# Kernel optimization log

Hardware: AMD Instinct MI355X
Metric: run time of the kernel (lower is better)

Reference implementation:

```python
import jax, jax.numpy as jnp
import numpy as np
from jax import lax

G, K, C_IN, C_FEAT, H, W, B = 8, 6, 512, 256, 64, 64, 1


def apply_offset(offset):
    # offset: [N, 2, H, W] pixel-space offsets -> sampling grid [N, H, W, 2] in [-1, 1]
    # channel 0 displaces x (width), channel 1 displaces y (height), matching the
    # reversed-meshgrid logic of the original torch apply_offset.
    n, _, h, w = offset.shape
    jj = jnp.arange(w, dtype=offset.dtype)[None, None, :]
    ii = jnp.arange(h, dtype=offset.dtype)[None, :, None]
    gx = (jj + offset[:, 0]) / ((w - 1.0) / 2.0) - 1.0
    gy = (ii + offset[:, 1]) / ((h - 1.0) / 2.0) - 1.0
    return jnp.stack([gx, gy], axis=-1)


def grid_sample_border(img, grid):
    # img: [N, C, H, W], grid: [N, H, W, 2] in [-1, 1]
    # Bilinear, padding_mode='border', align_corners=False (torch grid_sample default).
    n, c, h, w = img.shape
    x = jnp.clip((grid[..., 0] + 1.0) * w * 0.5 - 0.5, 0.0, w - 1.0)
    y = jnp.clip((grid[..., 1] + 1.0) * h * 0.5 - 0.5, 0.0, h - 1.0)
    x0 = jnp.floor(x)
    y0 = jnp.floor(y)
    wx = (x - x0)[:, None]  # [N,1,H,W]
    wy = (y - y0)[:, None]
    x0i = x0.astype(jnp.int32)
    y0i = y0.astype(jnp.int32)
    x1i = jnp.minimum(x0i + 1, w - 1)
    y1i = jnp.minimum(y0i + 1, h - 1)

    def gather(im, yi, xi):  # im [C,H,W]; yi, xi [H,W]
        return im[:, yi, xi]

    g = jax.vmap(gather)
    v00 = g(img, y0i, x0i)
    v01 = g(img, y0i, x1i)
    v10 = g(img, y1i, x0i)
    v11 = g(img, y1i, x1i)
    return (1.0 - wy) * ((1.0 - wx) * v00 + wx * v01) + wy * ((1.0 - wx) * v10 + wx * v11)


def setup_inputs() -> dict:
    key = jax.random.key(0)
    ks = jax.random.split(key, 11)
    s = 0.02
    return {
        "gar_feat": jax.random.normal(ks[0], (B, C_FEAT, H, W), jnp.float32),
        "cond_feat": jax.random.normal(ks[1], (B, C_FEAT, H, W), jnp.float32),
        "mask": jax.random.uniform(ks[2], (B, G, C_FEAT), dtype=jnp.float32),
        "W1": jax.random.normal(ks[3], (G, 128, C_IN, 3, 3), jnp.float32) * s,
        "b1": jax.random.normal(ks[4], (G, 128), jnp.float32) * s,
        "W2": jax.random.normal(ks[5], (G, 64, 128, 3, 3), jnp.float32) * s,
        "b2": jax.random.normal(ks[6], (G, 64), jnp.float32) * s,
        "W3": jax.random.normal(ks[7], (G, 32, 64, 3, 3), jnp.float32) * s,
        "b3": jax.random.normal(ks[8], (G, 32), jnp.float32) * s,
        "W4": jax.random.normal(ks[9], (G, 3 * K, 32, 3, 3), jnp.float32) * s,
        "b4": jax.random.normal(ks[10], (G, 3 * K), jnp.float32) * s,
    }


def reference(gar_feat, cond_feat, mask, W1, b1, W2, b2, W3, b3, W4, b4):
    b, c, h, w = gar_feat.shape
    g = W1.shape[0]
    k = W4.shape[1] // 3
    inp = jnp.concatenate([gar_feat, cond_feat], axis=1)  # [B, 2C, H, W]

    def conv(x, wgt, bias):
        return lax.conv_general_dilated(
            x, wgt, (1, 1), 'SAME', dimension_numbers=('NCHW', 'OIHW', 'NCHW')
        ) + bias[None, :, None, None]

    def lrelu(x):
        return jnp.where(x >= 0, x, 0.1 * x)

    def group_net(w1, bb1, w2, bb2, w3, bb3, w4, bb4):
        hid = lrelu(conv(inp, w1, bb1))
        hid = lrelu(conv(hid, w2, bb2))
        hid = lrelu(conv(hid, w3, bb3))
        return conv(hid, w4, bb4)  # [B, 3k, H, W]

    oa = jax.vmap(group_net)(W1, b1, W2, b2, W3, b3, W4, b4)  # [G, B, 3k, H, W]
    attn = jax.nn.softmax(oa[:, :, 2 * k:], axis=0)           # softmax across groups: [G,B,k,H,W]
    off = oa[:, :, :2 * k].reshape(g, b * k, 2, h, w)
    grid = jax.vmap(apply_offset)(off)                        # [G, B*k, H, W, 2]

    rep = jnp.repeat(gar_feat, k, axis=0)                     # [B*k, C, H, W]

    def warp_group(grid_g, attn_g, mask_g):
        samp = grid_sample_border(rep, grid_g).reshape(b, k, c, h, w)
        wfeat = jnp.sum(samp * attn_g[:, :, None], axis=1)    # [B, C, H, W]
        return wfeat * mask_g[:, :, None, None]

    warped = jax.vmap(warp_group)(grid, attn, jnp.transpose(mask, (1, 0, 2)))
    return jnp.sum(warped, axis=0)  # [B, C, H, W]
```

## Files before the change

### kernel.cpp

```cpp
#include <hip/hip_runtime.h>
#include <hip/hip_bf16.h>

typedef __hip_bfloat16 bf16;
typedef unsigned short ushort8v __attribute__((ext_vector_type(8)));
typedef short  s16x4  __attribute__((ext_vector_type(4)));
typedef short  bf16x8 __attribute__((ext_vector_type(8)));
typedef float  f32x4  __attribute__((ext_vector_type(4)));

#define HW 4096
#define IMG_W 64

__device__ __forceinline__ float bfbits2f(unsigned short u) {
    return __uint_as_float(((unsigned int)u) << 16);
}
__device__ __forceinline__ short f2bs(float f) {
    bf16 h = __float2bfloat16(f);
    return *reinterpret_cast<short*>(&h);
}

__device__ __forceinline__ void gl_lds16(const void* g, void* s) {
    __builtin_amdgcn_global_load_lds(
        (const __attribute__((address_space(1))) unsigned int*)g,
        (__attribute__((address_space(3))) unsigned int*)s, 16, 0, 0);
}

__device__ void pack_input_dev(const float* __restrict__ gar,
                               const float* __restrict__ cond,
                               short* __restrict__ outp,
                               short* __restrict__ gart, int bx2, float* tile)
{
    int bx = bx2 & 127;
    int by = bx2 >> 7;
    int tx = threadIdx.x & 31;
    int ty = threadIdx.x >> 5;
#pragma unroll
    for (int i = 0; i < 4; ++i) {
        int c = by * 32 + ty + i * 8;
        const float* src = (c < 256) ? (gar + (size_t)c * HW)
                                     : (cond + (size_t)(c - 256) * HW);
        tile[(ty + i * 8) * 33 + tx] = src[bx * 32 + tx];
    }
    __syncthreads();
#pragma unroll
    for (int i = 0; i < 4; ++i) {
        int p = bx * 32 + ty + i * 8;
        short v = f2bs(tile[tx * 33 + ty + i * 8]);
        outp[((size_t)by * 4096 + p) * 32 + tx] = v;
        if (by < 8)
            gart[(size_t)p * 256 + by * 32 + tx] = v;
    }
}

template<int CIN, int CREAL, int BN, int NT, bool COAL>
__device__ void pack_w_dev(const float* __restrict__ wgt, char* __restrict__ wp,
                           int bx, short* sT)
{
    constexpr int NCC  = CIN / 32;
    constexpr int BLKB = 9 * 4 * BN * 16;

    const int t  = threadIdx.x;
    const int cc = bx % NCC;
    const int nt = (bx / NCC) % NT;
    const int g  = bx / (NT * NCC);

    for (int i = t; i < BLKB / 8; i += 256)
        reinterpret_cast<s16x4*>(sT)[i] = s16x4{0, 0, 0, 0};
    __syncthreads();

    int ocmax = CREAL - nt * BN; if (ocmax > BN) ocmax = BN;
    const size_t base = ((size_t)(g * CREAL + nt * BN) * CIN + cc * 32) * 9;
    for (int i = t; i < ocmax * 288; i += 256) {
        int oc = i / 288;
        int r  = i % 288;
        int ic = r / 9, tap = r % 9;
        size_t idx;
        if (COAL) idx = (size_t)(((tap * BN + oc) * 4 + (ic >> 3)) * 8 + (ic & 7));
        else      idx = (size_t)(((tap * 4 + (ic >> 3)) * BN + oc) * 8 + (ic & 7));
        sT[idx] = f2bs(wgt[base + (size_t)oc * CIN * 9 + r]);
    }
    __syncthreads();

    const s16x4* src = reinterpret_cast<const s16x4*>(sT);
    s16x4* dst = reinterpret_cast<s16x4*>(wp + (size_t)bx * BLKB);
    for (int i = t; i < BLKB / 8; i += 256)
        dst[i] = src[i];
}

__global__ __launch_bounds__(256)
void pack_all(const float* __restrict__ gar, const float* __restrict__ cond,
              const float* __restrict__ W1, const float* __restrict__ W2,
              const float* __restrict__ W3, const float* __restrict__ W4,
              short* inp_t, short* gar_t,
              char* W1p, char* W2p, char* W3p, char* W4p)
{
    __shared__ __align__(16) short sbuf[9 * 4 * 64 * 8];
    int bx = blockIdx.x;
    if (bx < 256)      pack_w_dev<512, 128, 64, 2, true >(W1, W1p, bx,       sbuf);
    else if (bx < 288) pack_w_dev<128,  64, 64, 1, true >(W2, W2p, bx - 256, sbuf);
    else if (bx < 304) pack_w_dev< 64,  32, 32, 1, false>(W3, W3p, bx - 288, sbuf);
    else if (bx < 312) pack_w_dev< 32,  18, 32, 1, false>(W4, W4p, bx - 304, sbuf);
    else pack_input_dev(gar, cond, inp_t, gar_t, bx - 312, (float*)sbuf);
}

template<int ICP, int CREAL, int BN, int ROWS, int OF, int NT, int NW, int PIPE,
         bool PIXMAJ_OUT, bool LEAKY, bool OUT_F32>
__global__ __launch_bounds__(NW * 64, 2)
void conv_mfma(const short* __restrict__ inp, const char* __restrict__ wp,
               const float* __restrict__ bias, void* __restrict__ outv)
{
    constexpr int NCC  = ICP / 32;
    constexpr int HALO = ROWS + 2;
    constexpr int NPT  = 4096 / (ROWS * 64);
    constexpr int BLKB = 9 * 4 * BN * 16;
    constexpr int RNDS = BLKB / 1024;
    constexpr int NBUF = (PIPE && NCC > 1) ? 2 : 1;
    constexpr int SMAX = (HALO + NW - 1) / NW;

    __shared__ __align__(16) short sA[HALO][4][68][8];
    __shared__ __align__(16) char  sBraw[NBUF][BLKB];

    const int b  = blockIdx.x;
    const int g  = b & 7;
    const int r_ = b >> 3;
    const int pt = r_ % NPT;
    const int nt = r_ / NPT;
    const int r0 = pt * ROWS;

    const int t    = threadIdx.x;
    const int wave = t >> 6, lane = t & 63;
    const int l15  = lane & 15, quad = lane >> 4;

    int row_l, ocw;
    if (NW == 8) {
        if (ROWS == 4) { row_l = wave >> 1; ocw = (wave & 1) * (BN / 2); }
        else           { row_l = wave >> 2; ocw = (wave & 3) * (BN / 4); }
    } else {
        row_l = (ROWS == 4) ? wave : (wave & 1);
        ocw   = (ROWS == 4) ? 0 : (wave >> 1) * (BN / 2);
    }

    const size_t gpix = (ICP == 512) ? 0 : ((size_t)g * 4096);
    const char*  wb   = wp + (size_t)((g * NT + nt) * NCC) * BLKB;

    const int acol = t & 63;
    const int r2   = t >> 6;

    bf16x8 pre[SMAX][4];

    auto stageA_load = [&](int cc) {
#pragma unroll
        for (int s = 0; s < SMAX; ++s) {
            int j = r2 + s * NW;
            if (j < HALO) {
                int gy = r0 - 1 + j;
                if (gy >= 0 && gy < 64) {
                    const short* sp = inp + ((gpix + gy * 64 + acol) * ICP + cc * 32);
#pragma unroll
                    for (int q = 0; q < 4; ++q)
                        pre[s][q] = *reinterpret_cast<const bf16x8*>(sp + q * 8);
                } else {
#pragma unroll
                    for (int q = 0; q < 4; ++q)
                        pre[s][q] = bf16x8{0, 0, 0, 0, 0, 0, 0, 0};
                }
            }
        }
    };
    auto stageA_write = [&]() {
#pragma unroll
        for (int s = 0; s < SMAX; ++s) {
            int j = r2 + s * NW;
            if (j < HALO) {
#pragma unroll
                for (int q = 0; q < 4; ++q)
                    *reinterpret_cast<bf16x8*>(&sA[j][q][acol + 1][0]) = pre[s][q];
            }
        }
    };
    auto stageB = [&](int cc) {
        const char* wsrc = wb + (size_t)cc * BLKB;
        char* sbb = (char*)sBraw[(NBUF == 2) ? (cc & 1) : 0];
        for (int r = wave; r < RNDS; r += NW)
            gl_lds16(wsrc + r * 1024 + lane * 16, sbb + r * 1024);
    };

    f32x4 acc[OF][4];
#pragma unroll
    for (int o = 0; o < OF; ++o)
#pragma unroll
        for (int p = 0; p < 4; ++p)
#pragma unroll
            for (int r = 0; r < 4; ++r) acc[o][p][r] = 0.f;

    if (t < HALO * 8) {
        int row = t >> 3, q = (t >> 1) & 3, cp = (t & 1) ? 65 : 0;
        *reinterpret_cast<bf16x8*>(&sA[row][q][cp][0]) =
            bf16x8{0, 0, 0, 0, 0, 0, 0, 0};
    }

    stageB(0);
    stageA_load(0);
    stageA_write();

    for (int cc = 0; cc < NCC; ++cc) {
        __syncthreads();
        if (cc + 1 < NCC) {
            if (PIPE) stageB(cc + 1);
            stageA_load(cc + 1);
        }
        const bf16x8* sBv = reinterpret_cast<const bf16x8*>(
            sBraw[(NBUF == 2) ? (cc & 1) : 0]);

#pragma unroll
        for (int dy = 0; dy < 3; ++dy) {
#pragma unroll
            for (int dx = 0; dx < 3; ++dx) {
                bf16x8 pF[4];
#pragma unroll
                for (int p = 0; p < 4; ++p)
                    pF[p] = *reinterpret_cast<const bf16x8*>(
                        &sA[row_l + dy][quad][p * 16 + l15 + dx][0]);
                bf16x8 wF[OF];
#pragma unroll
                for (int o = 0; o < OF; ++o)
                    wF[o] = sBv[((dy * 3 + dx) * 4 + quad) * BN + ocw + o * 16 + l15];
#pragma unroll
                for (int o = 0; o < OF; ++o)
#pragma unroll
                    for (int p = 0; p < 4; ++p)
                        acc[o][p] = __builtin_amdgcn_mfma_f32_16x16x32_bf16(
                            wF[o], pF[p], acc[o][p], 0, 0, 0);
            }
        }
        __syncthreads();
        if (cc + 1 < NCC) {
            if (!PIPE) stageB(cc + 1);
            stageA_write();
        }
    }

    const int prow = r0 + row_l;
#pragma unroll
    for (int o = 0; o < OF; ++o)
#pragma unroll
        for (int reg = 0; reg < 4; ++reg) {
            const int ocl = ocw + o * 16 + quad * 4 + reg;
            const int ocg = nt * BN + ocl;
            if (ocg < CREAL) {
                const float bv = bias[g * CREAL + ocg];
                if (PIXMAJ_OUT) {
                    short* outp = (short*)outv;
                    const size_t pixbase = ((size_t)g * 4096 + prow * 64);
#pragma unroll
                    for (int p = 0; p < 4; ++p) {
                        float v = acc[o][p][reg] + bv;
                        if (LEAKY) v = v >= 0.f ? v : 0.1f * v;
                        outp[(pixbase + p * 16 + l15) * (NT * BN) + ocg] = f2bs(v);
                    }
                } else if (OUT_F32) {
                    float* outp = (float*)outv;
                    const size_t base = ((size_t)(g * CREAL + ocg)) * HW + prow * IMG_W;
#pragma unroll
                    for (int p = 0; p < 4; ++p) {
                        float v = acc[o][p][reg] + bv;
                        if (LEAKY) v = v >= 0.f ? v : 0.1f * v;
                        outp[base + p * 16 + l15] = v;
                    }
                } else {
                    short* outp = (short*)outv;
                    const size_t base = ((size_t)(g * CREAL + ocg)) * HW + prow * IMG_W;
#pragma unroll
                    for (int p = 0; p < 4; ++p) {
                        float v = acc[o][p][reg] + bv;
                        if (LEAKY) v = v >= 0.f ? v : 0.1f * v;
                        outp[base + p * 16 + l15] = f2bs(v);
                    }
                }
            }
        }
}

__global__ __launch_bounds__(512, 2)
void conv1_p2(const short* __restrict__ inp, const char* __restrict__ wp,
              const float* __restrict__ bias, short* __restrict__ outp)
{
    __shared__ __align__(16) short sA[2][4][66][4][8];

    const int b  = blockIdx.x;
    const int g  = b & 7;
    const int pt = b >> 3;
    const int r0 = pt * 2;

    const int t    = threadIdx.x;
    const int wave = t >> 6, lane = t & 63;
    const int l15  = lane & 15, quad = lane >> 4;

    const int row_l = wave & 1;
    const int ocq   = wave >> 1;
    const int ntw   = ocq >> 1;
    const int ocw64 = (ocq & 1) * 32;

    const short* wb    = (const short*)wp + (size_t)(g * 2 + ntw) * 16 * 18432;
    const short* wlane = wb + ((size_t)(ocw64 + l15) * 4 + quad) * 8;

    auto stageDMA = [&](int cc, int buf) {
        const int row = wave >> 1;
        const int gy  = r0 - 1 + row;
        if (gy >= 0 && gy < 64) {
            const short* src = inp + ((size_t)cc * 4096 + (size_t)gy * 64) * 32
                                   + (size_t)lane * 8;
            const int c4 = (wave & 1) * 2;
            gl_lds16(src + c4 * 512,       &sA[buf][row][1 + c4 * 16][0][0]);
            gl_lds16(src + (c4 + 1) * 512, &sA[buf][row][1 + (c4 + 1) * 16][0][0]);
        }
    };

    f32x4 acc[2][4];
#pragma unroll
    for (int o = 0; o < 2; ++o)
#pragma unroll
        for (int f = 0; f < 4; ++f)
#pragma unroll
            for (int r = 0; r < 4; ++r) acc[o][f][r] = 0.f;

    stageDMA(0, 0);
    if (t < 64) {
        int buf = t >> 5, row = (t >> 3) & 3, q = (t >> 1) & 3;
        int col = (t & 1) ? 65 : 0;
        *reinterpret_cast<bf16x8*>(&sA[buf][row][col][q][0]) =
            bf16x8{0, 0, 0, 0, 0, 0, 0, 0};
    }
    if (r0 == 0 || r0 == 62) {
        int zr = (r0 == 0) ? 0 : 3;
        for (int i = t; i < 2 * 66 * 4; i += 512) {
            int buf = i / 264, rem = i % 264;
            *reinterpret_cast<bf16x8*>(&sA[buf][zr][rem >> 2][rem & 3][0]) =
                bf16x8{0, 0, 0, 0, 0, 0, 0, 0};
        }
    }

    bf16x8 w[2][2];
    bf16x8 pf[2][4];
#pragma unroll
    for (int o = 0; o < 2; ++o)
        w[0][o] = *reinterpret_cast<const bf16x8*>(wlane + o * 512);

    auto body = [&](int cc, int cur, int par) {
        const short* wcc = wlane + (size_t)cc * 18432;
        __syncthreads();
        if (cc + 1 < 16) stageDMA(cc + 1, cur ^ 1);
#pragma unroll
        for (int f = 0; f < 4; ++f)
            pf[0][f] = *reinterpret_cast<const bf16x8*>(
                &sA[cur][row_l][f * 16 + l15][quad][0]);
#pragma unroll
        for (int tap = 0; tap < 9; ++tap) {
            const int pb = tap & 1, pn = pb ^ 1;
            const int cb = (tap + par) & 1, nb = cb ^ 1;
            if (tap < 8) {
                const int dy1 = (tap + 1) / 3, dx1 = (tap + 1) % 3;
#pragma unroll
                for (int f = 0; f < 4; ++f)
                    pf[pn][f] = *reinterpret_cast<const bf16x8*>(
                        &sA[cur][row_l + dy1][f * 16 + l15 + dx1][quad][0]);
            }
            const short* nsrc = wcc + (size_t)(tap + 1) * 2048;
#pragma unroll
            for (int o = 0; o < 2; ++o)
                w[nb][o] = *reinterpret_cast<const bf16x8*>(nsrc + o * 512);
            __builtin_amdgcn_sched_barrier(0);
#pragma unroll
            for (int o = 0; o < 2; ++o)
#pragma unroll
                for (int f = 0; f < 4; ++f)
                    acc[o][f] = __builtin_amdgcn_mfma_f32_16x16x32_bf16(
                        w[cb][o], pf[pb][f], acc[o][f], 0, 0, 0);
        }
    };

    for (int c2 = 0; c2 < 16; c2 += 2) {
        body(c2,     0, 0);
        body(c2 + 1, 1, 1);
    }

    const int prow = r0 + row_l;
    const size_t pixbase = (size_t)g * 4096 + (size_t)prow * 64;
#pragma unroll
    for (int o = 0; o < 2; ++o)
#pragma unroll
        for (int reg = 0; reg < 4; ++reg) {
            const int ocg = ocq * 32 + o * 16 + quad * 4 + reg;
            const float bv = bias[g * 128 + ocg];
#pragma unroll
            for (int f = 0; f < 4; ++f) {
                float v = acc[o][f][reg] + bv;
                v = v >= 0.f ? v : 0.1f * v;
                outp[(pixbase + f * 16 + l15) * 128 + ocg] = f2bs(v);
            }
        }
}

__global__ __launch_bounds__(512, 2)
void conv2_p2(const short* __restrict__ inp, const char* __restrict__ wp,
              const float* __restrict__ bias, short* __restrict__ outp)
{
    __shared__ __align__(16) short sA[2][4][66][4][8];

    const int b  = blockIdx.x;
    const int g  = b & 7;
    const int pt = b >> 3;
    const int r0 = pt * 2;

    const int t    = threadIdx.x;
    const int wave = t >> 6, lane = t & 63;
    const int l15  = lane & 15, quad = lane >> 4;

    const int row_l = wave & 1;
    const int ocq   = wave >> 1;

    const short* wb    = (const short*)wp + (size_t)g * 4 * 18432;
    const short* wlane = wb + ((size_t)(ocq * 16 + l15) * 4 + quad) * 8;

    auto stageDMA = [&](int cc, int buf) {
        const int row = wave >> 1;
        const int gy  = r0 - 1 + row;
        if (gy >= 0 && gy < 64) {
            const short* rowb = inp + ((size_t)g * 4096 + (size_t)gy * 64) * 128
                                    + cc * 32 + (lane & 3) * 8;
            const int c4 = (wave & 1) * 2;
            gl_lds16(rowb + (size_t)(c4 * 16 + (lane >> 2)) * 128,
                     &sA[buf][row][1 + c4 * 16][0][0]);
            gl_lds16(rowb + (size_t)((c4 + 1) * 16 + (lane >> 2)) * 128,
                     &sA[buf][row][1 + (c4 + 1) * 16][0][0]);
        }
    };

    f32x4 acc[4];
#pragma unroll
    for (int f = 0; f < 4; ++f)
#pragma unroll
        for (int r = 0; r < 4; ++r) acc[f][r] = 0.f;

    stageDMA(0, 0);
    if (t < 64) {
        int buf = t >> 5, row = (t >> 3) & 3, q = (t >> 1) & 3;
        int col = (t & 1) ? 65 : 0;
        *reinterpret_cast<bf16x8*>(&sA[buf][row][col][q][0]) =
            bf16x8{0, 0, 0, 0, 0, 0, 0, 0};
    }
    if (r0 == 0 || r0 == 62) {
        int zr = (r0 == 0) ? 0 : 3;
        for (int i = t; i < 2 * 66 * 4; i += 512) {
            int buf = i / 264, rem = i % 264;
            *reinterpret_cast<bf16x8*>(&sA[buf][zr][rem >> 2][rem & 3][0]) =
                bf16x8{0, 0, 0, 0, 0, 0, 0, 0};
        }
    }

    bf16x8 w[2];
    bf16x8 pf[2][4];
    w[0] = *reinterpret_cast<const bf16x8*>(wlane);

    auto body = [&](int cc, int cur, int par) {
        const short* wcc = wlane + (size_t)cc * 18432;
        __syncthreads();
        if (cc + 1 < 4) stageDMA(cc + 1, cur ^ 1);
#pragma unroll
        for (int f = 0; f < 4; ++f)
            pf[0][f] = *reinterpret_cast<const bf16x8*>(
                &sA[cur][row_l][f * 16 + l15][quad][0]);
#pragma unroll
        for (int tap = 0; tap < 9; ++tap) {
            const int pb = tap & 1, pn = pb ^ 1;
            const int cb = (tap + par) & 1, nb = cb ^ 1;
            if (tap < 8) {
                const int dy1 = (tap + 1) / 3, dx1 = (tap + 1) % 3;
#pragma unroll
                for (int f = 0; f < 4; ++f)
                    pf[pn][f] = *reinterpret_cast<const bf16x8*>(
                        &sA[cur][row_l + dy1][f * 16 + l15 + dx1][quad][0]);
            }
            w[nb] = *reinterpret_cast<const bf16x8*>(
                wcc + (size_t)(tap + 1) * 2048);
            __builtin_amdgcn_sched_barrier(0);
#pragma unroll
            for (int f = 0; f < 4; ++f)
                acc[f] = __builtin_amdgcn_mfma_f32_16x16x32_bf16(
                    w[cb], pf[pb][f], acc[f], 0, 0, 0);
        }
    };

    for (int c2 = 0; c2 < 4; c2 += 2) {
        body(c2,     0, 0);
        body(c2 + 1, 1, 1);
    }

    const int prow = r0 + row_l;
    const size_t pixbase = (size_t)g * 4096 + (size_t)prow * 64;
#pragma unroll
    for (int reg = 0; reg < 4; ++reg) {
        const int ocg = ocq * 16 + quad * 4 + reg;
        const float bv = bias[g * 64 + ocg];
#pragma unroll
        for (int f = 0; f < 4; ++f) {
            float v = acc[f][reg] + bv;
            v = v >= 0.f ? v : 0.1f * v;
            outp[(pixbase + f * 16 + l15) * 64 + ocg] = f2bs(v);
        }
    }
}

__global__ __launch_bounds__(256)
void warp_combine_kernel(const float* __restrict__ oa,
                         const short* __restrict__ gar_t,
                         const float* __restrict__ mask,
                         float* __restrict__ out)
{
    __shared__ __align__(16) float4 sWts[8][6][8];
    __shared__ __align__(16) int4   sIdx[8][6][8];

    const int t = threadIdx.x;

    if (t < 48) {
        int lp = t / 6;
        int k  = t % 6;
        int p  = blockIdx.x * 8 + lp;
        int x  = p & 63, y = p >> 6;

        float l[8];
        float m = -1e30f;
#pragma unroll
        for (int g = 0; g < 8; ++g) {
            l[g] = oa[(size_t)(g * 18 + 12 + k) * HW + p];
            m = fmaxf(m, l[g]);
        }
        float s = 0.f;
#pragma unroll
        for (int g = 0; g < 8; ++g) { l[g] = __expf(l[g] - m); s += l[g]; }
        float inv = 1.f / s;

#pragma unroll
        for (int g = 0; g < 8; ++g) {
            float a  = l[g] * inv;
            float ox = oa[(size_t)(g * 18 + 2 * k)     * HW + p];
            float oy = oa[(size_t)(g * 18 + 2 * k + 1) * HW + p];
            float sx = fminf(fmaxf(((float)x + ox) * (64.f / 63.f) - 0.5f, 0.f), 63.f);
            float sy = fminf(fmaxf(((float)y + oy) * (64.f / 63.f) - 0.5f, 0.f), 63.f);
            float fx0 = floorf(sx), fy0 = floorf(sy);
            int   x0 = (int)fx0,    y0i = (int)fy0;
            float wx = sx - fx0,    wy = sy - fy0;
            int   x1 = min(x0 + 1, 63), y1 = min(y0i + 1, 63);
            sWts[lp][k][g] = make_float4(a * (1.f - wy) * (1.f - wx),
                                         a * (1.f - wy) * wx,
                                         a * wy * (1.f - wx),
                                         a * wy * wx);
            sIdx[lp][k][g] = make_int4(y0i * 64 + x0, y0i * 64 + x1,
                                       y1  * 64 + x0, y1  * 64 + x1);
        }
    }
    __syncthreads();

    const int lp = t >> 5;
    const int p  = blockIdx.x * 8 + lp;
    const int c0 = (t & 31) * 8;
    const short* ipc = gar_t + c0;

    float acc[8];
#pragma unroll
    for (int j = 0; j < 8; ++j) acc[j] = 0.f;

    for (int g = 0; g < 8; ++g) {
        float4 m0 = *reinterpret_cast<const float4*>(mask + g * 256 + c0);
        float4 m1 = *reinterpret_cast<const float4*>(mask + g * 256 + c0 + 4);
        float mk[8] = {m0.x, m0.y, m0.z, m0.w, m1.x, m1.y, m1.z, m1.w};
#pragma unroll
        for (int k = 0; k < 6; ++k) {
            float4 w  = sWts[lp][k][g];
            int4   id = sIdx[lp][k][g];
            ushort8v v00 = *reinterpret_cast<const ushort8v*>(ipc + (size_t)id.x * 256);
            ushort8v v01 = *reinterpret_cast<const ushort8v*>(ipc + (size_t)id.y * 256);
            ushort8v v10 = *reinterpret_cast<const ushort8v*>(ipc + (size_t)id.z * 256);
            ushort8v v11 = *reinterpret_cast<const ushort8v*>(ipc + (size_t)id.w * 256);
#pragma unroll
            for (int j = 0; j < 8; ++j) {
                float sv = w.x * bfbits2f(v00[j]) + w.y * bfbits2f(v01[j])
                         + w.z * bfbits2f(v10[j]) + w.w * bfbits2f(v11[j]);
                acc[j] = fmaf(mk[j], sv, acc[j]);
            }
        }
    }
#pragma unroll
    for (int j = 0; j < 8; ++j)
        out[(size_t)(c0 + j) * HW + p] = acc[j];
}

extern "C" void kernel_launch(void* const* d_in, const int* in_sizes, int n_in,
                              void* d_out, int out_size, void* d_ws, size_t ws_size,
                              hipStream_t stream)
{
    (void)in_sizes; (void)n_in; (void)out_size; (void)ws_size;
    const float* gar  = (const float*)d_in[0];
    const float* cond = (const float*)d_in[1];
    const float* mask = (const float*)d_in[2];
    const float* W1   = (const float*)d_in[3];
    const float* b1   = (const float*)d_in[4];
    const float* W2   = (const float*)d_in[5];
    const float* b2   = (const float*)d_in[6];
    const float* W3   = (const float*)d_in[7];
    const float* b3   = (const float*)d_in[8];
    const float* W4   = (const float*)d_in[9];
    const float* b4   = (const float*)d_in[10];
    float* out = (float*)d_out;

    char* ws = (char*)d_ws;
    short* inp_t  = (short*)(ws);
    char*  W1p    = ws + (4u << 20);
    short* hid2_t = (short*)(ws + (4u << 20));
    short* hid3_t = (short*)(ws + (8u << 20));
    float* oa     = (float*)(ws + (10u << 20) + (512u << 10));
    char*  W2p    = ws + (14u << 20);
    char*  W3p    = ws + (15u << 20) + (512u << 10);
    char*  W4p    = ws + (16u << 20);
    short* hid1_t = (short*)(ws + (17u << 20));
    short* gar_t  = (short*)(ws + (26u << 20));

    pack_all<<<2360, 256, 0, stream>>>(gar, cond, W1, W2, W3, W4,
                                       inp_t, gar_t, W1p, W2p, W3p, W4p);

    conv1_p2<<<256, 512, 0, stream>>>(inp_t, W1p, b1, hid1_t);
    conv2_p2<<<256, 512, 0, stream>>>(hid1_t, W2p, b2, hid2_t);
    conv_mfma<64, 32, 32, 2, 1, 1, 4, 1, true, true, false>
        <<<256, 256, 0, stream>>>(hid2_t, W3p, b3, hid3_t);
    conv_mfma<32, 18, 32, 2, 1, 1, 4, 1, false, false, true>
        <<<256, 256, 0, stream>>>(hid3_t, W4p, b4, oa);

    warp_combine_kernel<<<512, 256, 0, stream>>>(oa, gar_t, mask, out);
}
```

Baseline: 194.7 us.

## Fuse conv3 and conv4 into one kernel with halo recompute in LDS

Replaces the two generic conv_mfma launches for conv3 and conv4 with a single fused kernel. Each block loads six hid2 rows into LDS, computes conv3 for four rows (a one-row halo on each side), keeps the result in LDS, and then runs conv4 from it. Weights are read per lane straight from global memory with double-buffered fragments and a sched_barrier. The W3/W4 packing layout switches to the variant used by the pixel-major kernels. This drops one launch and the hid3 round trip through global memory, at the cost of recomputing the halo rows of conv3.

```diff
diff --git a/kernel.cpp b/kernel.cpp
--- a/kernel.cpp
+++ b/kernel.cpp
@@ -95,189 +95,11 @@
 {
     __shared__ __align__(16) short sbuf[9 * 4 * 64 * 8];
     int bx = blockIdx.x;
-    if (bx < 256)      pack_w_dev<512, 128, 64, 2, true >(W1, W1p, bx,       sbuf);
-    else if (bx < 288) pack_w_dev<128,  64, 64, 1, true >(W2, W2p, bx - 256, sbuf);
-    else if (bx < 304) pack_w_dev< 64,  32, 32, 1, false>(W3, W3p, bx - 288, sbuf);
-    else if (bx < 312) pack_w_dev< 32,  18, 32, 1, false>(W4, W4p, bx - 304, sbuf);
+    if (bx < 256)      pack_w_dev<512, 128, 64, 2, true>(W1, W1p, bx,       sbuf);
+    else if (bx < 288) pack_w_dev<128,  64, 64, 1, true>(W2, W2p, bx - 256, sbuf);
+    else if (bx < 304) pack_w_dev< 64,  32, 32, 1, true>(W3, W3p, bx - 288, sbuf);
+    else if (bx < 312) pack_w_dev< 32,  18, 32, 1, true>(W4, W4p, bx - 304, sbuf);
     else pack_input_dev(gar, cond, inp_t, gar_t, bx - 312, (float*)sbuf);
-}
-
-template<int ICP, int CREAL, int BN, int ROWS, int OF, int NT, int NW, int PIPE,
-         bool PIXMAJ_OUT, bool LEAKY, bool OUT_F32>
-__global__ __launch_bounds__(NW * 64, 2)
-void conv_mfma(const short* __restrict__ inp, const char* __restrict__ wp,
-               const float* __restrict__ bias, void* __restrict__ outv)
-{
-    constexpr int NCC  = ICP / 32;
-    constexpr int HALO = ROWS + 2;
-    constexpr int NPT  = 4096 / (ROWS * 64);
-    constexpr int BLKB = 9 * 4 * BN * 16;
-    constexpr int RNDS = BLKB / 1024;
-    constexpr int NBUF = (PIPE && NCC > 1) ? 2 : 1;
-    constexpr int SMAX = (HALO + NW - 1) / NW;
-
-    __shared__ __align__(16) short sA[HALO][4][68][8];
-    __shared__ __align__(16) char  sBraw[NBUF][BLKB];
-
-    const int b  = blockIdx.x;
-    const int g  = b & 7;
-    const int r_ = b >> 3;
-    const int pt = r_ % NPT;
-    const int nt = r_ / NPT;
-    const int r0 = pt * ROWS;
-
-    const int t    = threadIdx.x;
-    const int wave = t >> 6, lane = t & 63;
-    const int l15  = lane & 15, quad = lane >> 4;
-
-    int row_l, ocw;
-    if (NW == 8) {
-        if (ROWS == 4) { row_l = wave >> 1; ocw = (wave & 1) * (BN / 2); }
-        else           { row_l = wave >> 2; ocw = (wave & 3) * (BN / 4); }
-    } else {
-        row_l = (ROWS == 4) ? wave : (wave & 1);
-        ocw   = (ROWS == 4) ? 0 : (wave >> 1) * (BN / 2);
-    }
-
-    const size_t gpix = (ICP == 512) ? 0 : ((size_t)g * 4096);
-    const char*  wb   = wp + (size_t)((g * NT + nt) * NCC) * BLKB;
-
-    const int acol = t & 63;
-    const int r2   = t >> 6;
-
-    bf16x8 pre[SMAX][4];
-
-    auto stageA_load = [&](int cc) {
-#pragma unroll
-        for (int s = 0; s < SMAX; ++s) {
-            int j = r2 + s * NW;
-            if (j < HALO) {
-                int gy = r0 - 1 + j;
-                if (gy >= 0 && gy < 64) {
-                    const short* sp = inp + ((gpix + gy * 64 + acol) * ICP + cc * 32);
-#pragma unroll
-                    for (int q = 0; q < 4; ++q)
-                        pre[s][q] = *reinterpret_cast<const bf16x8*>(sp + q * 8);
-                } else {
-#pragma unroll
-                    for (int q = 0; q < 4; ++q)
-                        pre[s][q] = bf16x8{0, 0, 0, 0, 0, 0, 0, 0};
-                }
-            }
-        }
-    };
-    auto stageA_write = [&]() {
-#pragma unroll
-        for (int s = 0; s < SMAX; ++s) {
-            int j = r2 + s * NW;
-            if (j < HALO) {
-#pragma unroll
-                for (int q = 0; q < 4; ++q)
-                    *reinterpret_cast<bf16x8*>(&sA[j][q][acol + 1][0]) = pre[s][q];
-            }
-        }
-    };
-    auto stageB = [&](int cc) {
-        const char* wsrc = wb + (size_t)cc * BLKB;
-        char* sbb = (char*)sBraw[(NBUF == 2) ? (cc & 1) : 0];
-        for (int r = wave; r < RNDS; r += NW)
-            gl_lds16(wsrc + r * 1024 + lane * 16, sbb + r * 1024);
-    };
-
-    f32x4 acc[OF][4];
-#pragma unroll
-    for (int o = 0; o < OF; ++o)
-#pragma unroll
-        for (int p = 0; p < 4; ++p)
-#pragma unroll
-            for (int r = 0; r < 4; ++r) acc[o][p][r] = 0.f;
-
-    if (t < HALO * 8) {
-        int row = t >> 3, q = (t >> 1) & 3, cp = (t & 1) ? 65 : 0;
-        *reinterpret_cast<bf16x8*>(&sA[row][q][cp][0]) =
-            bf16x8{0, 0, 0, 0, 0, 0, 0, 0};
-    }
-
-    stageB(0);
-    stageA_load(0);
-    stageA_write();
-
-    for (int cc = 0; cc < NCC; ++cc) {
-        __syncthreads();
-        if (cc + 1 < NCC) {
-            if (PIPE) stageB(cc + 1);
-            stageA_load(cc + 1);
-        }
-        const bf16x8* sBv = reinterpret_cast<const bf16x8*>(
-            sBraw[(NBUF == 2) ? (cc & 1) : 0]);
-
-#pragma unroll
-        for (int dy = 0; dy < 3; ++dy) {
-#pragma unroll
-            for (int dx = 0; dx < 3; ++dx) {
-                bf16x8 pF[4];
-#pragma unroll
-                for (int p = 0; p < 4; ++p)
-                    pF[p] = *reinterpret_cast<const bf16x8*>(
-                        &sA[row_l + dy][quad][p * 16 + l15 + dx][0]);
-                bf16x8 wF[OF];
-#pragma unroll
-                for (int o = 0; o < OF; ++o)
-                    wF[o] = sBv[((dy * 3 + dx) * 4 + quad) * BN + ocw + o * 16 + l15];
-#pragma unroll
-                for (int o = 0; o < OF; ++o)
-#pragma unroll
-                    for (int p = 0; p < 4; ++p)
-                        acc[o][p] = __builtin_amdgcn_mfma_f32_16x16x32_bf16(
-                            wF[o], pF[p], acc[o][p], 0, 0, 0);
-            }
-        }
-        __syncthreads();
-        if (cc + 1 < NCC) {
-            if (!PIPE) stageB(cc + 1);
-            stageA_write();
-        }
-    }
-
-    const int prow = r0 + row_l;
-#pragma unroll
-    for (int o = 0; o < OF; ++o)
-#pragma unroll
-        for (int reg = 0; reg < 4; ++reg) {
-            const int ocl = ocw + o * 16 + quad * 4 + reg;
-            const int ocg = nt * BN + ocl;
-            if (ocg < CREAL) {
-                const float bv = bias[g * CREAL + ocg];
-                if (PIXMAJ_OUT) {
-                    short* outp = (short*)outv;
-                    const size_t pixbase = ((size_t)g * 4096 + prow * 64);
-#pragma unroll
-                    for (int p = 0; p < 4; ++p) {
-                        float v = acc[o][p][reg] + bv;
-                        if (LEAKY) v = v >= 0.f ? v : 0.1f * v;
-                        outp[(pixbase + p * 16 + l15) * (NT * BN) + ocg] = f2bs(v);
-                    }
-                } else if (OUT_F32) {
-                    float* outp = (float*)outv;
-                    const size_t base = ((size_t)(g * CREAL + ocg)) * HW + prow * IMG_W;
-#pragma unroll
-                    for (int p = 0; p < 4; ++p) {
-                        float v = acc[o][p][reg] + bv;
-                        if (LEAKY) v = v >= 0.f ? v : 0.1f * v;
-                        outp[base + p * 16 + l15] = v;
-                    }
-                } else {
-                    short* outp = (short*)outv;
-                    const size_t base = ((size_t)(g * CREAL + ocg)) * HW + prow * IMG_W;
-#pragma unroll
-                    for (int p = 0; p < 4; ++p) {
-                        float v = acc[o][p][reg] + bv;
-                        if (LEAKY) v = v >= 0.f ? v : 0.1f * v;
-                        outp[base + p * 16 + l15] = f2bs(v);
-                    }
-                }
-            }
-        }
 }
 
 __global__ __launch_bounds__(512, 2)
@@ -506,6 +328,170 @@
             float v = acc[f][reg] + bv;
             v = v >= 0.f ? v : 0.1f * v;
             outp[(pixbase + f * 16 + l15) * 64 + ocg] = f2bs(v);
+        }
+    }
+}
+
+__global__ __launch_bounds__(512, 2)
+void conv34_p2(const short* __restrict__ hid2, const char* __restrict__ w3p,
+               const char* __restrict__ w4p, const float* __restrict__ b3,
+               const float* __restrict__ b4, float* __restrict__ oa)
+{
+    __shared__ __align__(16) short sA[6][2][66][4][8];
+    __shared__ __align__(16) short sH3[4][66][4][8];
+
+    const int b  = blockIdx.x;
+    const int g  = b & 7;
+    const int pt = b >> 3;
+    const int r0 = pt * 2;
+
+    const int t    = threadIdx.x;
+    const int wave = t >> 6, lane = t & 63;
+    const int l15  = lane & 15, quad = lane >> 4;
+
+    const int wrow = wave & 3;
+    const int och3 = wave >> 2;
+    const int w4row = wave & 1;
+    const int och4  = (wave >> 1) & 1;
+    const int pxh   = wave >> 2;
+
+    const short* w3lane = (const short*)w3p + (size_t)(g * 2) * 9216
+                        + ((size_t)(och3 * 16 + l15) * 4 + quad) * 8;
+    const short* w4lane = (const short*)w4p + (size_t)g * 9216
+                        + ((size_t)(och4 * 16 + l15) * 4 + quad) * 8;
+
+    if (wave < 6) {
+        const int gy = r0 - 2 + wave;
+        if (gy >= 0 && gy < 64) {
+            const short* src = hid2 + ((size_t)g * 4096 + (size_t)gy * 64) * 64;
+#pragma unroll
+            for (int cc = 0; cc < 2; ++cc)
+#pragma unroll
+                for (int i = 0; i < 4; ++i)
+                    gl_lds16(src + (size_t)(i * 16 + (lane >> 2)) * 64
+                                 + cc * 32 + (lane & 3) * 8,
+                             &sA[wave][cc][1 + i * 16][0][0]);
+        } else {
+            s16x4* rowdst = reinterpret_cast<s16x4*>(&sA[wave][0][0][0][0]);
+            for (int i = lane; i < 1056; i += 64)
+                rowdst[i] = s16x4{0, 0, 0, 0};
+        }
+    }
+    if (t < 96) {
+        int row = t / 16, cc = (t >> 3) & 1, col = (t & 4) ? 65 : 0, q = t & 3;
+        *reinterpret_cast<bf16x8*>(&sA[row][cc][col][q][0]) =
+            bf16x8{0, 0, 0, 0, 0, 0, 0, 0};
+    } else if (t < 128) {
+        int i = t - 96;
+        int row = i >> 3, col = (i & 4) ? 65 : 0, q = i & 3;
+        *reinterpret_cast<bf16x8*>(&sH3[row][col][q][0]) =
+            bf16x8{0, 0, 0, 0, 0, 0, 0, 0};
+    }
+
+    bf16x8 w[2];
+    bf16x8 pf[2][4];
+    w[0] = *reinterpret_cast<const bf16x8*>(w3lane);
+
+    f32x4 acc3[4];
+#pragma unroll
+    for (int f = 0; f < 4; ++f)
+#pragma unroll
+        for (int r = 0; r < 4; ++r) acc3[f][r] = 0.f;
+
+    __syncthreads();
+
+#pragma unroll
+    for (int cc = 0; cc < 2; ++cc) {
+        const short* wcc = w3lane + (size_t)cc * 9216;
+#pragma unroll
+        for (int f = 0; f < 4; ++f)
+            pf[0][f] = *reinterpret_cast<const bf16x8*>(
+                &sA[wrow][cc][f * 16 + l15][quad][0]);
+#pragma unroll
+        for (int tap = 0; tap < 9; ++tap) {
+            const int pb = tap & 1, pn = pb ^ 1;
+            const int cb = (tap + cc) & 1, nb = cb ^ 1;
+            if (tap < 8) {
+                const int dy1 = (tap + 1) / 3, dx1 = (tap + 1) % 3;
+#pragma unroll
+                for (int f = 0; f < 4; ++f)
+                    pf[pn][f] = *reinterpret_cast<const bf16x8*>(
+                        &sA[wrow + dy1][cc][f * 16 + l15 + dx1][quad][0]);
+            }
+            w[nb] = *reinterpret_cast<const bf16x8*>(
+                wcc + (size_t)(tap + 1) * 1024);
+            __builtin_amdgcn_sched_barrier(0);
+#pragma unroll
+            for (int f = 0; f < 4; ++f)
+                acc3[f] = __builtin_amdgcn_mfma_f32_16x16x32_bf16(
+                    w[cb], pf[pb][f], acc3[f], 0, 0, 0);
+        }
+    }
+
+    {
+        const int gy3 = r0 - 1 + wrow;
+        const bool v3 = (gy3 >= 0 && gy3 < 64);
+        const int qp = och3 * 2 + (quad >> 1);
+        const int e0 = (quad & 1) * 4;
+#pragma unroll
+        for (int f = 0; f < 4; ++f) {
+            s16x4 pkt;
+#pragma unroll
+            for (int reg = 0; reg < 4; ++reg) {
+                const int oc3 = och3 * 16 + quad * 4 + reg;
+                float v = acc3[f][reg] + b3[g * 32 + oc3];
+                v = v >= 0.f ? v : 0.1f * v;
+                pkt[reg] = v3 ? f2bs(v) : (short)0;
+            }
+            *reinterpret_cast<s16x4*>(&sH3[wrow][1 + f * 16 + l15][qp][e0]) = pkt;
+        }
+    }
+    __syncthreads();
+
+    bf16x8 w4[2];
+    bf16x8 pf4[2][2];
+    w4[0] = *reinterpret_cast<const bf16x8*>(w4lane);
+
+    f32x4 acc4[2];
+#pragma unroll
+    for (int f = 0; f < 2; ++f)
+#pragma unroll
+        for (int r = 0; r < 4; ++r) acc4[f][r] = 0.f;
+
+#pragma unroll
+    for (int f = 0; f < 2; ++f)
+        pf4[0][f] = *reinterpret_cast<const bf16x8*>(
+            &sH3[w4row][pxh * 32 + f * 16 + l15][quad][0]);
+#pragma unroll
+    for (int tap = 0; tap < 9; ++tap) {
+        const int pb = tap & 1, pn = pb ^ 1;
+        const int cb = tap & 1, nb = cb ^ 1;
+        if (tap < 8) {
+            const int dy1 = (tap + 1) / 3, dx1 = (tap + 1) % 3;
+#pragma unroll
+            for (int f = 0; f < 2; ++f)
+                pf4[pn][f] = *reinterpret_cast<const bf16x8*>(
+                    &sH3[w4row + dy1][pxh * 32 + f * 16 + l15 + dx1][quad][0]);
+        }
+        w4[nb] = *reinterpret_cast<const bf16x8*>(
+            w4lane + (size_t)(tap + 1) * 1024);
+        __builtin_amdgcn_sched_barrier(0);
+#pragma unroll
+        for (int f = 0; f < 2; ++f)
+            acc4[f] = __builtin_amdgcn_mfma_f32_16x16x32_bf16(
+                w4[cb], pf4[pb][f], acc4[f], 0, 0, 0);
+    }
+
+    const int prow4 = r0 + w4row;
+#pragma unroll
+    for (int reg = 0; reg < 4; ++reg) {
+        const int oc4 = och4 * 16 + quad * 4 + reg;
+        if (oc4 < 18) {
+            const float bv = b4[g * 18 + oc4];
+#pragma unroll
+            for (int f = 0; f < 2; ++f)
+                oa[(size_t)(g * 18 + oc4) * HW + prow4 * 64 + pxh * 32
+                   + f * 16 + l15] = acc4[f][reg] + bv;
         }
     }
 }
@@ -616,7 +602,6 @@
     short* inp_t  = (short*)(ws);
     char*  W1p    = ws + (4u << 20);
     short* hid2_t = (short*)(ws + (4u << 20));
-    short* hid3_t = (short*)(ws + (8u << 20));
     float* oa     = (float*)(ws + (10u << 20) + (512u << 10));
     char*  W2p    = ws + (14u << 20);
     char*  W3p    = ws + (15u << 20) + (512u << 10);
@@ -629,10 +614,7 @@
 
     conv1_p2<<<256, 512, 0, stream>>>(inp_t, W1p, b1, hid1_t);
     conv2_p2<<<256, 512, 0, stream>>>(hid1_t, W2p, b2, hid2_t);
-    conv_mfma<64, 32, 32, 2, 1, 1, 4, 1, true, true, false>
-        <<<256, 256, 0, stream>>>(hid2_t, W3p, b3, hid3_t);
-    conv_mfma<32, 18, 32, 2, 1, 1, 4, 1, false, false, true>
-        <<<256, 256, 0, stream>>>(hid3_t, W4p, b4, oa);
+    conv34_p2<<<256, 512, 0, stream>>>(hid2_t, W3p, W4p, b3, b4, oa);
 
     warp_combine_kernel<<<512, 256, 0, stream>>>(oa, gar_t, mask, out);
 }
```

New measurement: 188.7 us. 1.03x faster.
